# Kernel tuning notes

Measured on AMD Instinct MI355X. Metric: run time of the kernel, lower is better.

Reference implementation:

```python
import jax, jax.numpy as jnp
import numpy as np

N_USERS = 100000
N_ITEMS = 400000
N_NODES = N_USERS + N_ITEMS
EMB_DIM = 64
N_LAYERS = 3
N_EDGES = 1200000


def setup_inputs() -> dict:
    key = jax.random.key(0)
    k1, k2, k3, k4 = jax.random.split(key, 4)
    # Xavier-uniform init for embedding tables
    bound_u = float(np.sqrt(6.0 / (N_USERS + EMB_DIM)))
    bound_i = float(np.sqrt(6.0 / (N_ITEMS + EMB_DIM)))
    user_emb_w = jax.random.uniform(k1, (N_USERS, EMB_DIM), jnp.float32, -bound_u, bound_u)
    item_emb_w = jax.random.uniform(k2, (N_ITEMS, EMB_DIM), jnp.float32, -bound_i, bound_i)
    edge_index = jax.random.randint(k3, (2, N_EDGES), 0, N_NODES, dtype=jnp.int64)
    edge_weight = jax.random.uniform(k4, (N_EDGES,), jnp.float32)
    return {
        "user_emb_w": user_emb_w,
        "item_emb_w": item_emb_w,
        "edge_index": edge_index,
        "edge_weight": edge_weight,
    }


def _lgconv(x, src, dst, w):
    # gather source features, scale by edge weight, scatter-add to dst
    msgs = x[src] * w[:, None]              # [E, D]
    return jax.ops.segment_sum(msgs, dst, num_segments=N_NODES)  # [N, D]


def reference(user_emb_w, item_emb_w, edge_index, edge_weight):
    src, dst = edge_index[0], edge_index[1]
    x = jnp.concatenate([user_emb_w, item_emb_w], axis=0)  # [N, D]
    acc = x  # running sum of layer embeddings (fused stack+mean)
    for _ in range(N_LAYERS):
        x = _lgconv(x, src, dst, edge_weight)
        acc = acc + x
    final = acc / jnp.asarray(N_LAYERS + 1, x.dtype)
    return final[:N_USERS], final[N_USERS:]
```

## Files before the change

### kernel.cpp

```cpp
#include <hip/hip_runtime.h>

#define N_USERS 100000
#define N_ITEMS 400000
#define N_NODES 500000
#define EMB_DIM 64
#define N_EDGES 1200000

#define BUCK_SHIFT 11
#define BUCK_NODES 2048
#define NBUCK 245
#define BUCK_CAP 6144
#define CHUNK 4096

typedef long long ll;
typedef float f4 __attribute__((ext_vector_type(4)));
typedef float f8 __attribute__((ext_vector_type(8)));
typedef unsigned short u16;
typedef u16 us8 __attribute__((ext_vector_type(8)));

__device__ __forceinline__ u16 f2bf(float f) {
    unsigned u = __float_as_uint(f);
    u += 0x7FFF + ((u >> 16) & 1);
    return (u16)(u >> 16);
}
__device__ __forceinline__ float bf2f(u16 h) {
    return __uint_as_float(((unsigned)h) << 16);
}
__device__ __forceinline__ void fma8(f8& s, float w, us8 v) {
    #pragma unroll
    for (int k = 0; k < 8; ++k) s[k] += w * bf2f(v[k]);
}


__global__ void k_init(int* __restrict__ gcur) {
    if (threadIdx.x < 256) gcur[threadIdx.x] = 0;
}

__global__ void k_bsort(const int* __restrict__ src, const int* __restrict__ dst,
                        const float* __restrict__ w,
                        int* __restrict__ gcur, uint2* __restrict__ stage) {
    __shared__ int lhist[256];
    __shared__ int gbase_s[256];
    __shared__ int lcur[256];
    int tid = threadIdx.x;
    lhist[tid] = 0;
    __syncthreads();
    int c0 = blockIdx.x * CHUNK;
    int c1 = c0 + CHUNK < N_EDGES ? c0 + CHUNK : N_EDGES;
    #pragma unroll
    for (int r = 0; r < CHUNK / 256; ++r) {
        int e = c0 + r * 256 + tid;
        if (e < c1) atomicAdd(&lhist[dst[e] >> BUCK_SHIFT], 1);
    }
    __syncthreads();
    if (tid < NBUCK) {
        gbase_s[tid] = atomicAdd(&gcur[tid], lhist[tid]);
        lcur[tid] = 0;
    }
    __syncthreads();
    #pragma unroll
    for (int r = 0; r < CHUNK / 256; ++r) {
        int e = c0 + r * 256 + tid;
        if (e < c1) {
            int s = src[e];
            int d = dst[e];
            float wt = w[e];
            int b = d >> BUCK_SHIFT;
            int k = atomicAdd(&lcur[b], 1);
            ll idx = (ll)b * BUCK_CAP + gbase_s[b] + k;
            stage[idx] = make_uint2((unsigned)s | ((unsigned)(d & (BUCK_NODES - 1)) << 19),
                                    __float_as_uint(wt));
        }
    }
}

__global__ void k_ncount(const uint2* __restrict__ stage, const int* __restrict__ gcur,
                         int* __restrict__ counts) {
    __shared__ int lh[BUCK_NODES];
    int b = blockIdx.x;
    int tid = threadIdx.x;
    #pragma unroll
    for (int r = 0; r < BUCK_NODES / 256; ++r) lh[r * 256 + tid] = 0;
    __syncthreads();
    int cnt = gcur[b];
    const uint2* sb = stage + (ll)b * BUCK_CAP;
    for (int i = tid; i < cnt; i += 256)
        atomicAdd(&lh[(sb[i].x >> 19) & (BUCK_NODES - 1)], 1);
    __syncthreads();
    int nbase = b * BUCK_NODES;
    #pragma unroll
    for (int r = 0; r < BUCK_NODES / 256; ++r) {
        int i = r * 256 + tid;
        int n = nbase + i;
        if (n < N_NODES) counts[n] = lh[i];
    }
}

#define SCAN_ELEMS 1024
__global__ void k_scan1(int* __restrict__ data, int* __restrict__ blocksums) {
    __shared__ int tmp[256];
    int b = blockIdx.x;
    int t = threadIdx.x;
    int base = b * SCAN_ELEMS + t * 4;
    int v[4];
    #pragma unroll
    for (int k = 0; k < 4; ++k) {
        int i = base + k;
        v[k] = (i < N_NODES) ? data[i] : 0;
    }
    int tsum = v[0] + v[1] + v[2] + v[3];
    tmp[t] = tsum;
    __syncthreads();
    for (int off = 1; off < 256; off <<= 1) {
        int x = (t >= off) ? tmp[t - off] : 0;
        __syncthreads();
        tmp[t] += x;
        __syncthreads();
    }
    int run = tmp[t] - tsum;
    #pragma unroll
    for (int k = 0; k < 4; ++k) {
        int i = base + k;
        if (i < N_NODES) data[i] = run;
        run += v[k];
    }
    if (t == 255) blocksums[b] = tmp[255];
}

__global__ void k_scan2(int* __restrict__ blocksums, int nb) {
    __shared__ int tmp[512];
    int t = threadIdx.x;
    int v = (t < nb) ? blocksums[t] : 0;
    tmp[t] = v;
    __syncthreads();
    for (int off = 1; off < 512; off <<= 1) {
        int x = (t >= off) ? tmp[t - off] : 0;
        __syncthreads();
        tmp[t] += x;
        __syncthreads();
    }
    if (t < nb) blocksums[t] = tmp[t] - v;
}

__global__ void k_scan3(int* __restrict__ rowptr, const int* __restrict__ blocksums) {
    int stride = gridDim.x * blockDim.x;
    for (int i = blockIdx.x * blockDim.x + threadIdx.x; i < N_NODES; i += stride)
        rowptr[i] = rowptr[i] + blocksums[i >> 10];
    if (blockIdx.x == 0 && threadIdx.x == 0) rowptr[N_NODES] = N_EDGES;
}

__global__ void k_place(const uint2* __restrict__ stage, const int* __restrict__ gcur,
                        const int* __restrict__ rowptr, int2* __restrict__ csr) {
    __shared__ int lpos[BUCK_NODES];
    int b = blockIdx.x;
    int tid = threadIdx.x;
    int nbase = b * BUCK_NODES;
    #pragma unroll
    for (int r = 0; r < BUCK_NODES / 256; ++r) {
        int i = r * 256 + tid;
        int n = nbase + i;
        lpos[i] = (n < N_NODES) ? rowptr[n] : 0;
    }
    __syncthreads();
    int cnt = gcur[b];
    const uint2* sb = stage + (ll)b * BUCK_CAP;
    for (int i = tid; i < cnt; i += 256) {
        uint2 e = sb[i];
        int ldst = (e.x >> 19) & (BUCK_NODES - 1);
        int s = e.x & 0x7FFFF;
        int pos = atomicAdd(&lpos[ldst], 1);
        csr[pos] = make_int2(s, (int)e.y);
    }
}


__global__ void k_conv(const f4* __restrict__ u4, const f4* __restrict__ i4,
                       us8* __restrict__ x0b) {
    const int total = N_NODES * 8;
    const int user8 = N_USERS * 8;
    int stride = gridDim.x * blockDim.x;
    for (int i = blockIdx.x * blockDim.x + threadIdx.x; i < total; i += stride) {
        const f4* p = (i < user8) ? (u4 + (ll)i * 2) : (i4 + (ll)(i - user8) * 2);
        f4 lo = __builtin_nontemporal_load(p);
        f4 hi = __builtin_nontemporal_load(p + 1);
        us8 o;
        #pragma unroll
        for (int k = 0; k < 4; ++k) { o[k] = f2bf(lo[k]); o[k + 4] = f2bf(hi[k]); }
        x0b[i] = o;
    }
}


__device__ __forceinline__ f8 gather8(const us8* __restrict__ xin,
                                      const int* __restrict__ rowptr,
                                      const int2* __restrict__ csr,
                                      int n, int fl) {
    int start = rowptr[n];
    int end   = rowptr[n + 1];
    int deg = end - start;
    f8 s = {0.f, 0.f, 0.f, 0.f, 0.f, 0.f, 0.f, 0.f};
    if (deg > 0) {
        int lastj = end - 1;
        int j1 = start + 1 < end ? start + 1 : lastj;
        int j2 = start + 2 < end ? start + 2 : lastj;
        int j3 = start + 3 < end ? start + 3 : lastj;
        int2 e0 = csr[start];
        int2 e1 = csr[j1];
        int2 e2 = csr[j2];
        int2 e3 = csr[j3];
        float w0 = __int_as_float(e0.y);
        float w1 = (deg > 1) ? __int_as_float(e1.y) : 0.f;
        float w2 = (deg > 2) ? __int_as_float(e2.y) : 0.f;
        float w3 = (deg > 3) ? __int_as_float(e3.y) : 0.f;
        us8 v0 = xin[(ll)e0.x * 8 + fl];
        us8 v1 = xin[(ll)e1.x * 8 + fl];
        us8 v2 = xin[(ll)e2.x * 8 + fl];
        us8 v3 = xin[(ll)e3.x * 8 + fl];
        fma8(s, w0, v0);
        fma8(s, w1, v1);
        fma8(s, w2, v2);
        fma8(s, w3, v3);
        int j = start + 4;
        for (; j + 1 < end; j += 2) {
            int2 a = csr[j];
            int2 b = csr[j + 1];
            us8 va = xin[(ll)a.x * 8 + fl];
            us8 vb = xin[(ll)b.x * 8 + fl];
            fma8(s, __int_as_float(a.y), va);
            fma8(s, __int_as_float(b.y), vb);
        }
        if (j < end) {
            int2 a = csr[j];
            us8 va = xin[(ll)a.x * 8 + fl];
            fma8(s, __int_as_float(a.y), va);
        }
    }
    return s;
}

__global__ void k_prop(const us8* __restrict__ xin,
                       const int* __restrict__ rowptr,
                       const int2* __restrict__ csr,
                       us8* __restrict__ xout) {
    int wave = (blockIdx.x * blockDim.x + threadIdx.x) >> 6;
    int lane = threadIdx.x & 63;
    int sub = lane >> 3;
    int fl  = lane & 7;
    int nwaves = (gridDim.x * blockDim.x) >> 6;
    for (int nb = wave * 8; nb < N_NODES; nb += nwaves * 8) {
        int n = nb + sub;
        f8 s = gather8(xin, rowptr, csr, n, fl);
        us8 o;
        #pragma unroll
        for (int k = 0; k < 8; ++k) o[k] = f2bf(s[k]);
        xout[(ll)n * 8 + fl] = o;
    }
}

__global__ void k_final(const us8* __restrict__ x0b,
                        const us8* __restrict__ x1b, const us8* __restrict__ x2b,
                        const int* __restrict__ rowptr,
                        const int2* __restrict__ csr,
                        f4* __restrict__ acc) {
    int wave = (blockIdx.x * blockDim.x + threadIdx.x) >> 6;
    int lane = threadIdx.x & 63;
    int sub = lane >> 3;
    int fl  = lane & 7;
    int nwaves = (gridDim.x * blockDim.x) >> 6;
    for (int nb = wave * 8; nb < N_NODES; nb += nwaves * 8) {
        int n = nb + sub;
        f8 s = gather8(x2b, rowptr, csr, n, fl);
        ll idx8 = (ll)n * 8 + fl;
        us8 x0v = x0b[idx8];
        us8 x1v = __builtin_nontemporal_load(&x1b[idx8]);
        us8 x2v = x2b[idx8];
        f4 rlo, rhi;
        #pragma unroll
        for (int k = 0; k < 4; ++k)
            rlo[k] = 0.25f * (bf2f(x0v[k]) + bf2f(x1v[k]) + bf2f(x2v[k]) + s[k]);
        #pragma unroll
        for (int k = 0; k < 4; ++k)
            rhi[k] = 0.25f * (bf2f(x0v[k + 4]) + bf2f(x1v[k + 4]) + bf2f(x2v[k + 4]) + s[k + 4]);
        f4* arow = acc + (ll)n * 16;
        __builtin_nontemporal_store(rlo, &arow[fl * 2]);
        __builtin_nontemporal_store(rhi, &arow[fl * 2 + 1]);
    }
}


__global__ void fb_init(const float* __restrict__ user_w,
                        const float* __restrict__ item_w,
                        float* __restrict__ acc, float* __restrict__ xcur) {
    const ll total4 = (ll)N_NODES * EMB_DIM / 4;
    const ll user4 = (ll)N_USERS * EMB_DIM / 4;
    const float4* uw = (const float4*)user_w;
    const float4* iw = (const float4*)item_w;
    float4* a4 = (float4*)acc;
    float4* x4 = (float4*)xcur;
    ll stride = (ll)gridDim.x * blockDim.x;
    for (ll i = (ll)blockIdx.x * blockDim.x + threadIdx.x; i < total4; i += stride) {
        float4 v = (i < user4) ? uw[i] : iw[i - user4];
        x4[i] = v;
        a4[i] = make_float4(0.25f * v.x, 0.25f * v.y, 0.25f * v.z, 0.25f * v.w);
    }
}
__global__ void fb_zero(float* __restrict__ p) {
    const ll total4 = (ll)N_NODES * EMB_DIM / 4;
    float4* p4 = (float4*)p;
    ll stride = (ll)gridDim.x * blockDim.x;
    float4 z = make_float4(0.f, 0.f, 0.f, 0.f);
    for (ll i = (ll)blockIdx.x * blockDim.x + threadIdx.x; i < total4; i += stride)
        p4[i] = z;
}
__global__ void fb_scatter(const float* __restrict__ xcur, const int* __restrict__ src,
                           const int* __restrict__ dst, const float* __restrict__ w,
                           float* __restrict__ xnext) {
    const int gpb = blockDim.x >> 6;
    const int d = threadIdx.x & 63;
    int eg = blockIdx.x * gpb + (threadIdx.x >> 6);
    const int estride = gridDim.x * gpb;
    for (int e = eg; e < N_EDGES; e += estride) {
        int s = src[e]; int t = dst[e]; float wt = w[e];
        atomicAdd(&xnext[(ll)t * EMB_DIM + d], xcur[(ll)s * EMB_DIM + d] * wt);
    }
}
__global__ void fb_accadd(const float* __restrict__ xn, float* __restrict__ acc) {
    const ll total4 = (ll)N_NODES * EMB_DIM / 4;
    const float4* x4 = (const float4*)xn;
    float4* a4 = (float4*)acc;
    ll stride = (ll)gridDim.x * blockDim.x;
    for (ll i = (ll)blockIdx.x * blockDim.x + threadIdx.x; i < total4; i += stride) {
        float4 v = x4[i]; float4 a = a4[i];
        a.x += 0.25f * v.x; a.y += 0.25f * v.y;
        a.z += 0.25f * v.z; a.w += 0.25f * v.w;
        a4[i] = a;
    }
}


extern "C" void kernel_launch(void* const* d_in, const int* in_sizes, int n_in,
                              void* d_out, int out_size, void* d_ws, size_t ws_size,
                              hipStream_t stream) {
    const float* user_w = (const float*)d_in[0];
    const float* item_w = (const float*)d_in[1];
    const int*   eidx   = (const int*)d_in[2];
    const float* ew     = (const float*)d_in[3];
    const int* src = eidx;
    const int* dst = eidx + N_EDGES;

    const size_t xb_bf = (size_t)N_NODES * EMB_DIM * 2;
    size_t off = 0;
    size_t x0_off     = off;   off += xb_bf;
    size_t x1_off     = off;   off += xb_bf;
    size_t x2_off     = off;   off += xb_bf;
    size_t stage_off  = off;   off += (size_t)NBUCK * BUCK_CAP * 8;
    size_t csr_off    = off;   off += (size_t)N_EDGES * 8;
    size_t rowptr_off = off;   off += (size_t)(N_NODES + 1) * 4;
    size_t gcur_off   = off;   off += 256 * 4;
    size_t bsums_off  = off;   off += 4096;
    const size_t need = off;

    const int blk = 256;

    if (ws_size >= need) {
        us8*   x0b   = (us8*)((char*)d_ws + x0_off);
        us8*   x1b   = (us8*)((char*)d_ws + x1_off);
        us8*   x2b   = (us8*)((char*)d_ws + x2_off);
        uint2* stage = (uint2*)((char*)d_ws + stage_off);
        int2*  csr   = (int2*)((char*)d_ws + csr_off);
        int*   rowptr = (int*)((char*)d_ws + rowptr_off);
        int*   gcur   = (int*)((char*)d_ws + gcur_off);
        int*   bsums  = (int*)((char*)d_ws + bsums_off);
        f4*    acc    = (f4*)d_out;
        const f4* u4 = (const f4*)user_w;
        const f4* i4 = (const f4*)item_w;

        const int nb_scan = (N_NODES + SCAN_ELEMS - 1) / SCAN_ELEMS;
        const int nb_sort = (N_EDGES + CHUNK - 1) / CHUNK;

        k_init<<<1, 256, 0, stream>>>(gcur);
        k_bsort<<<nb_sort, blk, 0, stream>>>(src, dst, ew, gcur, stage);
        k_ncount<<<NBUCK, blk, 0, stream>>>(stage, gcur, rowptr);
        k_scan1<<<nb_scan, 256, 0, stream>>>(rowptr, bsums);
        k_scan2<<<1, 512, 0, stream>>>(bsums, nb_scan);
        k_scan3<<<2048, blk, 0, stream>>>(rowptr, bsums);
        k_place<<<NBUCK, blk, 0, stream>>>(stage, gcur, rowptr, csr);

        k_conv<<<2048, blk, 0, stream>>>(u4, i4, x0b);

        const int grid_l = 4096;
        k_prop<<<grid_l, blk, 0, stream>>>(x0b, rowptr, csr, x1b);
        k_prop<<<grid_l, blk, 0, stream>>>(x1b, rowptr, csr, x2b);
        k_final<<<grid_l, blk, 0, stream>>>(x0b, x1b, x2b, rowptr, csr, acc);
    } else {
        float* acc = (float*)d_out;
        float* xcur = (float*)d_ws;
        float* xnext = xcur + (ll)N_NODES * EMB_DIM;
        fb_init<<<2048, blk, 0, stream>>>(user_w, item_w, acc, xcur);
        for (int layer = 0; layer < 3; ++layer) {
            fb_zero<<<2048, blk, 0, stream>>>(xnext);
            fb_scatter<<<4096, blk, 0, stream>>>(xcur, src, dst, ew, xnext);
            fb_accadd<<<2048, blk, 0, stream>>>(xnext, acc);
            float* tmp = xcur; xcur = xnext; xnext = tmp;
        }
    }
}
```

Measured before the change: 244.1 us.

## Fuse embedding conversion into bucket sort and process two nodes per sub-wave

The fp32-to-bf16 conversion of the embedding tables now runs in extra blocks of the bucket-sort kernel, so the two independent jobs share one launch and can overlap. The propagation and final kernels now handle two destination nodes per 8-lane group, issuing the first four neighbour gathers for both nodes up front. This raises memory-level parallelism in the latency-bound gather and removes one launch. In exchange it uses more registers per thread, which may lower occupancy, and it adds clamped speculative CSR index loads.

```diff
diff --git a/kernel.cpp b/kernel.cpp
--- a/kernel.cpp
+++ b/kernel.cpp
@@ -11,6 +11,8 @@
 #define NBUCK 245
 #define BUCK_CAP 6144
 #define CHUNK 4096
+#define NB_SORT 293
+#define NB_CONV 1024
 
 typedef long long ll;
 typedef float f4 __attribute__((ext_vector_type(4)));
@@ -36,13 +38,33 @@
     if (threadIdx.x < 256) gcur[threadIdx.x] = 0;
 }
 
-__global__ void k_bsort(const int* __restrict__ src, const int* __restrict__ dst,
-                        const float* __restrict__ w,
-                        int* __restrict__ gcur, uint2* __restrict__ stage) {
+__global__ void k_bsort_conv(const int* __restrict__ src, const int* __restrict__ dst,
+                             const float* __restrict__ w,
+                             int* __restrict__ gcur, uint2* __restrict__ stage,
+                             const f4* __restrict__ u4, const f4* __restrict__ i4,
+                             us8* __restrict__ x0b) {
     __shared__ int lhist[256];
     __shared__ int gbase_s[256];
     __shared__ int lcur[256];
     int tid = threadIdx.x;
+
+    if (blockIdx.x >= NB_SORT) {
+        const int total = N_NODES * 8;
+        const int user8 = N_USERS * 8;
+        int i0 = (blockIdx.x - NB_SORT) * 256 + tid;
+        int stride = NB_CONV * 256;
+        for (int i = i0; i < total; i += stride) {
+            const f4* p = (i < user8) ? (u4 + (ll)i * 2) : (i4 + (ll)(i - user8) * 2);
+            f4 lo = __builtin_nontemporal_load(p);
+            f4 hi = __builtin_nontemporal_load(p + 1);
+            us8 o;
+            #pragma unroll
+            for (int k = 0; k < 4; ++k) { o[k] = f2bf(lo[k]); o[k + 4] = f2bf(hi[k]); }
+            x0b[i] = o;
+        }
+        return;
+    }
+
     lhist[tid] = 0;
     __syncthreads();
     int c0 = blockIdx.x * CHUNK;
@@ -174,68 +196,32 @@
 }
 
 
-__global__ void k_conv(const f4* __restrict__ u4, const f4* __restrict__ i4,
-                       us8* __restrict__ x0b) {
-    const int total = N_NODES * 8;
-    const int user8 = N_USERS * 8;
-    int stride = gridDim.x * blockDim.x;
-    for (int i = blockIdx.x * blockDim.x + threadIdx.x; i < total; i += stride) {
-        const f4* p = (i < user8) ? (u4 + (ll)i * 2) : (i4 + (ll)(i - user8) * 2);
-        f4 lo = __builtin_nontemporal_load(p);
-        f4 hi = __builtin_nontemporal_load(p + 1);
-        us8 o;
-        #pragma unroll
-        for (int k = 0; k < 4; ++k) { o[k] = f2bf(lo[k]); o[k + 4] = f2bf(hi[k]); }
-        x0b[i] = o;
-    }
-}
-
-
-__device__ __forceinline__ f8 gather8(const us8* __restrict__ xin,
-                                      const int* __restrict__ rowptr,
-                                      const int2* __restrict__ csr,
-                                      int n, int fl) {
-    int start = rowptr[n];
-    int end   = rowptr[n + 1];
-    int deg = end - start;
-    f8 s = {0.f, 0.f, 0.f, 0.f, 0.f, 0.f, 0.f, 0.f};
-    if (deg > 0) {
-        int lastj = end - 1;
-        int j1 = start + 1 < end ? start + 1 : lastj;
-        int j2 = start + 2 < end ? start + 2 : lastj;
-        int j3 = start + 3 < end ? start + 3 : lastj;
-        int2 e0 = csr[start];
-        int2 e1 = csr[j1];
-        int2 e2 = csr[j2];
-        int2 e3 = csr[j3];
-        float w0 = __int_as_float(e0.y);
-        float w1 = (deg > 1) ? __int_as_float(e1.y) : 0.f;
-        float w2 = (deg > 2) ? __int_as_float(e2.y) : 0.f;
-        float w3 = (deg > 3) ? __int_as_float(e3.y) : 0.f;
-        us8 v0 = xin[(ll)e0.x * 8 + fl];
-        us8 v1 = xin[(ll)e1.x * 8 + fl];
-        us8 v2 = xin[(ll)e2.x * 8 + fl];
-        us8 v3 = xin[(ll)e3.x * 8 + fl];
-        fma8(s, w0, v0);
-        fma8(s, w1, v1);
-        fma8(s, w2, v2);
-        fma8(s, w3, v3);
-        int j = start + 4;
-        for (; j + 1 < end; j += 2) {
-            int2 a = csr[j];
-            int2 b = csr[j + 1];
-            us8 va = xin[(ll)a.x * 8 + fl];
-            us8 vb = xin[(ll)b.x * 8 + fl];
-            fma8(s, __int_as_float(a.y), va);
-            fma8(s, __int_as_float(b.y), vb);
-        }
-        if (j < end) {
-            int2 a = csr[j];
-            us8 va = xin[(ll)a.x * 8 + fl];
-            fma8(s, __int_as_float(a.y), va);
-        }
-    }
-    return s;
+__device__ __forceinline__ void bidx4(int start, int end,
+                                      int& j0, int& j1, int& j2, int& j3) {
+    j0 = start < N_EDGES - 1 ? start : N_EDGES - 1;
+    int lastj = (end - 1 > start) ? end - 1 : j0;
+    j1 = start + 1 < end ? start + 1 : lastj;
+    j2 = start + 2 < end ? start + 2 : lastj;
+    j3 = start + 3 < end ? start + 3 : lastj;
+}
+
+__device__ __forceinline__ void rem4(const us8* __restrict__ xin,
+                                     const int2* __restrict__ csr,
+                                     int start, int end, int fl, f8& s) {
+    int j = start + 4;
+    for (; j + 1 < end; j += 2) {
+        int2 a = csr[j];
+        int2 b = csr[j + 1];
+        us8 va = xin[(ll)a.x * 8 + fl];
+        us8 vb = xin[(ll)b.x * 8 + fl];
+        fma8(s, __int_as_float(a.y), va);
+        fma8(s, __int_as_float(b.y), vb);
+    }
+    if (j < end) {
+        int2 a = csr[j];
+        us8 va = xin[(ll)a.x * 8 + fl];
+        fma8(s, __int_as_float(a.y), va);
+    }
 }
 
 __global__ void k_prop(const us8* __restrict__ xin,
@@ -247,13 +233,46 @@
     int sub = lane >> 3;
     int fl  = lane & 7;
     int nwaves = (gridDim.x * blockDim.x) >> 6;
-    for (int nb = wave * 8; nb < N_NODES; nb += nwaves * 8) {
-        int n = nb + sub;
-        f8 s = gather8(xin, rowptr, csr, n, fl);
-        us8 o;
+    for (int nb = wave * 16; nb < N_NODES; nb += nwaves * 16) {
+        int na = nb + sub;
+        int nc = nb + 8 + sub;
+        int sa = rowptr[na], ea = rowptr[na + 1];
+        int sc = rowptr[nc], ec = rowptr[nc + 1];
+        int dega = ea - sa, degc = ec - sc;
+        int ja0, ja1, ja2, ja3, jc0, jc1, jc2, jc3;
+        bidx4(sa, ea, ja0, ja1, ja2, ja3);
+        bidx4(sc, ec, jc0, jc1, jc2, jc3);
+        int2 a0 = csr[ja0], a1 = csr[ja1], a2 = csr[ja2], a3 = csr[ja3];
+        int2 c0 = csr[jc0], c1 = csr[jc1], c2 = csr[jc2], c3 = csr[jc3];
+        us8 va0 = xin[(ll)a0.x * 8 + fl];
+        us8 va1 = xin[(ll)a1.x * 8 + fl];
+        us8 va2 = xin[(ll)a2.x * 8 + fl];
+        us8 va3 = xin[(ll)a3.x * 8 + fl];
+        us8 vc0 = xin[(ll)c0.x * 8 + fl];
+        us8 vc1 = xin[(ll)c1.x * 8 + fl];
+        us8 vc2 = xin[(ll)c2.x * 8 + fl];
+        us8 vc3 = xin[(ll)c3.x * 8 + fl];
+        float wa0 = (dega > 0) ? __int_as_float(a0.y) : 0.f;
+        float wa1 = (dega > 1) ? __int_as_float(a1.y) : 0.f;
+        float wa2 = (dega > 2) ? __int_as_float(a2.y) : 0.f;
+        float wa3 = (dega > 3) ? __int_as_float(a3.y) : 0.f;
+        float wc0 = (degc > 0) ? __int_as_float(c0.y) : 0.f;
+        float wc1 = (degc > 1) ? __int_as_float(c1.y) : 0.f;
+        float wc2 = (degc > 2) ? __int_as_float(c2.y) : 0.f;
+        float wc3 = (degc > 3) ? __int_as_float(c3.y) : 0.f;
+        f8 s1 = {0.f, 0.f, 0.f, 0.f, 0.f, 0.f, 0.f, 0.f};
+        f8 s2 = {0.f, 0.f, 0.f, 0.f, 0.f, 0.f, 0.f, 0.f};
+        fma8(s1, wa0, va0); fma8(s1, wa1, va1);
+        fma8(s1, wa2, va2); fma8(s1, wa3, va3);
+        fma8(s2, wc0, vc0); fma8(s2, wc1, vc1);
+        fma8(s2, wc2, vc2); fma8(s2, wc3, vc3);
+        if (dega > 4) rem4(xin, csr, sa, ea, fl, s1);
+        if (degc > 4) rem4(xin, csr, sc, ec, fl, s2);
+        us8 o1, o2;
         #pragma unroll
-        for (int k = 0; k < 8; ++k) o[k] = f2bf(s[k]);
-        xout[(ll)n * 8 + fl] = o;
+        for (int k = 0; k < 8; ++k) { o1[k] = f2bf(s1[k]); o2[k] = f2bf(s2[k]); }
+        xout[(ll)na * 8 + fl] = o1;
+        xout[(ll)nc * 8 + fl] = o2;
     }
 }
 
@@ -267,21 +286,64 @@
     int sub = lane >> 3;
     int fl  = lane & 7;
     int nwaves = (gridDim.x * blockDim.x) >> 6;
-    for (int nb = wave * 8; nb < N_NODES; nb += nwaves * 8) {
-        int n = nb + sub;
-        f8 s = gather8(x2b, rowptr, csr, n, fl);
-        ll idx8 = (ll)n * 8 + fl;
-        us8 x0v = x0b[idx8];
-        us8 x1v = __builtin_nontemporal_load(&x1b[idx8]);
-        us8 x2v = x2b[idx8];
+    for (int nb = wave * 16; nb < N_NODES; nb += nwaves * 16) {
+        int na = nb + sub;
+        int nc = nb + 8 + sub;
+        int sa = rowptr[na], ea = rowptr[na + 1];
+        int sc = rowptr[nc], ec = rowptr[nc + 1];
+        int dega = ea - sa, degc = ec - sc;
+        int ja0, ja1, ja2, ja3, jc0, jc1, jc2, jc3;
+        bidx4(sa, ea, ja0, ja1, ja2, ja3);
+        bidx4(sc, ec, jc0, jc1, jc2, jc3);
+        int2 a0 = csr[ja0], a1 = csr[ja1], a2 = csr[ja2], a3 = csr[ja3];
+        int2 c0 = csr[jc0], c1 = csr[jc1], c2 = csr[jc2], c3 = csr[jc3];
+        ll ia = (ll)na * 8 + fl;
+        ll ic = (ll)nc * 8 + fl;
+        us8 va0 = x2b[(ll)a0.x * 8 + fl];
+        us8 va1 = x2b[(ll)a1.x * 8 + fl];
+        us8 va2 = x2b[(ll)a2.x * 8 + fl];
+        us8 va3 = x2b[(ll)a3.x * 8 + fl];
+        us8 vc0 = x2b[(ll)c0.x * 8 + fl];
+        us8 vc1 = x2b[(ll)c1.x * 8 + fl];
+        us8 vc2 = x2b[(ll)c2.x * 8 + fl];
+        us8 vc3 = x2b[(ll)c3.x * 8 + fl];
+        us8 x0a = x0b[ia];
+        us8 x1a = __builtin_nontemporal_load(&x1b[ia]);
+        us8 x2a = x2b[ia];
+        us8 x0c = x0b[ic];
+        us8 x1c = __builtin_nontemporal_load(&x1b[ic]);
+        us8 x2c = x2b[ic];
+        float wa0 = (dega > 0) ? __int_as_float(a0.y) : 0.f;
+        float wa1 = (dega > 1) ? __int_as_float(a1.y) : 0.f;
+        float wa2 = (dega > 2) ? __int_as_float(a2.y) : 0.f;
+        float wa3 = (dega > 3) ? __int_as_float(a3.y) : 0.f;
+        float wc0 = (degc > 0) ? __int_as_float(c0.y) : 0.f;
+        float wc1 = (degc > 1) ? __int_as_float(c1.y) : 0.f;
+        float wc2 = (degc > 2) ? __int_as_float(c2.y) : 0.f;
+        float wc3 = (degc > 3) ? __int_as_float(c3.y) : 0.f;
+        f8 s1 = {0.f, 0.f, 0.f, 0.f, 0.f, 0.f, 0.f, 0.f};
+        f8 s2 = {0.f, 0.f, 0.f, 0.f, 0.f, 0.f, 0.f, 0.f};
+        fma8(s1, wa0, va0); fma8(s1, wa1, va1);
+        fma8(s1, wa2, va2); fma8(s1, wa3, va3);
+        fma8(s2, wc0, vc0); fma8(s2, wc1, vc1);
+        fma8(s2, wc2, vc2); fma8(s2, wc3, vc3);
+        if (dega > 4) rem4(x2b, csr, sa, ea, fl, s1);
+        if (degc > 4) rem4(x2b, csr, sc, ec, fl, s2);
         f4 rlo, rhi;
         #pragma unroll
-        for (int k = 0; k < 4; ++k)
-            rlo[k] = 0.25f * (bf2f(x0v[k]) + bf2f(x1v[k]) + bf2f(x2v[k]) + s[k]);
+        for (int k = 0; k < 4; ++k) {
+            rlo[k] = 0.25f * (bf2f(x0a[k]) + bf2f(x1a[k]) + bf2f(x2a[k]) + s1[k]);
+            rhi[k] = 0.25f * (bf2f(x0a[k + 4]) + bf2f(x1a[k + 4]) + bf2f(x2a[k + 4]) + s1[k + 4]);
+        }
+        f4* arow = acc + (ll)na * 16;
+        __builtin_nontemporal_store(rlo, &arow[fl * 2]);
+        __builtin_nontemporal_store(rhi, &arow[fl * 2 + 1]);
         #pragma unroll
-        for (int k = 0; k < 4; ++k)
-            rhi[k] = 0.25f * (bf2f(x0v[k + 4]) + bf2f(x1v[k + 4]) + bf2f(x2v[k + 4]) + s[k + 4]);
-        f4* arow = acc + (ll)n * 16;
+        for (int k = 0; k < 4; ++k) {
+            rlo[k] = 0.25f * (bf2f(x0c[k]) + bf2f(x1c[k]) + bf2f(x2c[k]) + s2[k]);
+            rhi[k] = 0.25f * (bf2f(x0c[k + 4]) + bf2f(x1c[k + 4]) + bf2f(x2c[k + 4]) + s2[k + 4]);
+        }
+        arow = acc + (ll)nc * 16;
         __builtin_nontemporal_store(rlo, &arow[fl * 2]);
         __builtin_nontemporal_store(rhi, &arow[fl * 2 + 1]);
     }
@@ -376,17 +438,15 @@
         const f4* i4 = (const f4*)item_w;
 
         const int nb_scan = (N_NODES + SCAN_ELEMS - 1) / SCAN_ELEMS;
-        const int nb_sort = (N_EDGES + CHUNK - 1) / CHUNK;
 
         k_init<<<1, 256, 0, stream>>>(gcur);
-        k_bsort<<<nb_sort, blk, 0, stream>>>(src, dst, ew, gcur, stage);
+        k_bsort_conv<<<NB_SORT + NB_CONV, blk, 0, stream>>>(src, dst, ew, gcur,
+                                                            stage, u4, i4, x0b);
         k_ncount<<<NBUCK, blk, 0, stream>>>(stage, gcur, rowptr);
         k_scan1<<<nb_scan, 256, 0, stream>>>(rowptr, bsums);
         k_scan2<<<1, 512, 0, stream>>>(bsums, nb_scan);
         k_scan3<<<2048, blk, 0, stream>>>(rowptr, bsums);
         k_place<<<NBUCK, blk, 0, stream>>>(stage, gcur, rowptr, csr);
-
-        k_conv<<<2048, blk, 0, stream>>>(u4, i4, x0b);
 
         const int grid_l = 4096;
         k_prop<<<grid_l, blk, 0, stream>>>(x0b, rowptr, csr, x1b);
```

Result: faster. 237.0 us (-2.9%).

## Fuse CSR build stages and merge bf16 conversion into bucket sort kernel

Applied to the files above, without the earlier changes.

Folds the float-to-bf16 embedding conversion into the bucket-sort launch as extra blocks, and replaces the global per-node count plus three-kernel scan with a tiny bucket-level scan followed by a per-bucket local histogram/scan inside the placement kernel. The second propagation layer now also writes the partial accumulator (x0+x1+x2), so the final kernel only reads acc and adds its own gather. This removes several launches and full passes over the 500k-entry rowptr array. In exchange the final kernel does a read-modify-write of the fp32 output instead of reading two bf16 arrays, and the mid layer writes fp32 output it did not write before.

```diff
diff --git a/kernel.cpp b/kernel.cpp
--- a/kernel.cpp
+++ b/kernel.cpp
@@ -11,6 +11,8 @@
 #define NBUCK 245
 #define BUCK_CAP 6144
 #define CHUNK 4096
+#define NB_SORT 293
+#define NB_CONV 1024
 
 typedef long long ll;
 typedef float f4 __attribute__((ext_vector_type(4)));
@@ -36,13 +38,33 @@
     if (threadIdx.x < 256) gcur[threadIdx.x] = 0;
 }
 
-__global__ void k_bsort(const int* __restrict__ src, const int* __restrict__ dst,
-                        const float* __restrict__ w,
-                        int* __restrict__ gcur, uint2* __restrict__ stage) {
+__global__ void k_bsort_conv(const int* __restrict__ src, const int* __restrict__ dst,
+                             const float* __restrict__ w,
+                             int* __restrict__ gcur, uint2* __restrict__ stage,
+                             const f4* __restrict__ u4, const f4* __restrict__ i4,
+                             us8* __restrict__ x0b) {
     __shared__ int lhist[256];
     __shared__ int gbase_s[256];
     __shared__ int lcur[256];
     int tid = threadIdx.x;
+
+    if (blockIdx.x >= NB_SORT) {
+        const int total = N_NODES * 8;
+        const int user8 = N_USERS * 8;
+        int i0 = (blockIdx.x - NB_SORT) * 256 + tid;
+        int stride = NB_CONV * 256;
+        for (int i = i0; i < total; i += stride) {
+            const f4* p = (i < user8) ? (u4 + (ll)i * 2) : (i4 + (ll)(i - user8) * 2);
+            f4 lo = __builtin_nontemporal_load(p);
+            f4 hi = __builtin_nontemporal_load(p + 1);
+            us8 o;
+            #pragma unroll
+            for (int k = 0; k < 4; ++k) { o[k] = f2bf(lo[k]); o[k + 4] = f2bf(hi[k]); }
+            x0b[i] = o;
+        }
+        return;
+    }
+
     lhist[tid] = 0;
     __syncthreads();
     int c0 = blockIdx.x * CHUNK;
@@ -74,42 +96,12 @@
     }
 }
 
-__global__ void k_ncount(const uint2* __restrict__ stage, const int* __restrict__ gcur,
-                         int* __restrict__ counts) {
-    __shared__ int lh[BUCK_NODES];
-    int b = blockIdx.x;
-    int tid = threadIdx.x;
-    #pragma unroll
-    for (int r = 0; r < BUCK_NODES / 256; ++r) lh[r * 256 + tid] = 0;
-    __syncthreads();
-    int cnt = gcur[b];
-    const uint2* sb = stage + (ll)b * BUCK_CAP;
-    for (int i = tid; i < cnt; i += 256)
-        atomicAdd(&lh[(sb[i].x >> 19) & (BUCK_NODES - 1)], 1);
-    __syncthreads();
-    int nbase = b * BUCK_NODES;
-    #pragma unroll
-    for (int r = 0; r < BUCK_NODES / 256; ++r) {
-        int i = r * 256 + tid;
-        int n = nbase + i;
-        if (n < N_NODES) counts[n] = lh[i];
-    }
-}
-
-#define SCAN_ELEMS 1024
-__global__ void k_scan1(int* __restrict__ data, int* __restrict__ blocksums) {
+__global__ void k_bscan(const int* __restrict__ gcur, int* __restrict__ bbase,
+                        int* __restrict__ rowptr) {
     __shared__ int tmp[256];
-    int b = blockIdx.x;
     int t = threadIdx.x;
-    int base = b * SCAN_ELEMS + t * 4;
-    int v[4];
-    #pragma unroll
-    for (int k = 0; k < 4; ++k) {
-        int i = base + k;
-        v[k] = (i < N_NODES) ? data[i] : 0;
-    }
-    int tsum = v[0] + v[1] + v[2] + v[3];
-    tmp[t] = tsum;
+    int v = (t < NBUCK) ? gcur[t] : 0;
+    tmp[t] = v;
     __syncthreads();
     for (int off = 1; off < 256; off <<= 1) {
         int x = (t >= off) ? tmp[t - off] : 0;
@@ -117,76 +109,54 @@
         tmp[t] += x;
         __syncthreads();
     }
-    int run = tmp[t] - tsum;
-    #pragma unroll
-    for (int k = 0; k < 4; ++k) {
-        int i = base + k;
-        if (i < N_NODES) data[i] = run;
-        run += v[k];
-    }
-    if (t == 255) blocksums[b] = tmp[255];
-}
-
-__global__ void k_scan2(int* __restrict__ blocksums, int nb) {
-    __shared__ int tmp[512];
-    int t = threadIdx.x;
-    int v = (t < nb) ? blocksums[t] : 0;
-    tmp[t] = v;
-    __syncthreads();
-    for (int off = 1; off < 512; off <<= 1) {
-        int x = (t >= off) ? tmp[t - off] : 0;
-        __syncthreads();
-        tmp[t] += x;
-        __syncthreads();
-    }
-    if (t < nb) blocksums[t] = tmp[t] - v;
-}
-
-__global__ void k_scan3(int* __restrict__ rowptr, const int* __restrict__ blocksums) {
-    int stride = gridDim.x * blockDim.x;
-    for (int i = blockIdx.x * blockDim.x + threadIdx.x; i < N_NODES; i += stride)
-        rowptr[i] = rowptr[i] + blocksums[i >> 10];
-    if (blockIdx.x == 0 && threadIdx.x == 0) rowptr[N_NODES] = N_EDGES;
-}
-
-__global__ void k_place(const uint2* __restrict__ stage, const int* __restrict__ gcur,
-                        const int* __restrict__ rowptr, int2* __restrict__ csr) {
-    __shared__ int lpos[BUCK_NODES];
+    if (t < NBUCK) bbase[t] = tmp[t] - v;
+    if (t == 0) rowptr[N_NODES] = N_EDGES;
+}
+
+__global__ void k_place2(const uint2* __restrict__ stage, const int* __restrict__ gcur,
+                         const int* __restrict__ bbase,
+                         int* __restrict__ rowptr, int2* __restrict__ csr) {
+    __shared__ int lh[BUCK_NODES];
+    __shared__ int tsum[256];
     int b = blockIdx.x;
     int tid = threadIdx.x;
-    int nbase = b * BUCK_NODES;
-    #pragma unroll
-    for (int r = 0; r < BUCK_NODES / 256; ++r) {
-        int i = r * 256 + tid;
-        int n = nbase + i;
-        lpos[i] = (n < N_NODES) ? rowptr[n] : 0;
-    }
+    #pragma unroll
+    for (int r = 0; r < BUCK_NODES / 256; ++r) lh[r * 256 + tid] = 0;
     __syncthreads();
     int cnt = gcur[b];
     const uint2* sb = stage + (ll)b * BUCK_CAP;
+    for (int i = tid; i < cnt; i += 256)
+        atomicAdd(&lh[(sb[i].x >> 19) & (BUCK_NODES - 1)], 1);
+    __syncthreads();
+    int base_t = tid * 8;
+    int v[8];
+    int s = 0;
+    #pragma unroll
+    for (int k = 0; k < 8; ++k) { v[k] = lh[base_t + k]; s += v[k]; }
+    tsum[tid] = s;
+    __syncthreads();
+    for (int off = 1; off < 256; off <<= 1) {
+        int x = (tid >= off) ? tsum[tid - off] : 0;
+        __syncthreads();
+        tsum[tid] += x;
+        __syncthreads();
+    }
+    int run = bbase[b] + tsum[tid] - s;
+    int nbase = b * BUCK_NODES;
+    #pragma unroll
+    for (int k = 0; k < 8; ++k) {
+        int i = base_t + k;
+        int n = nbase + i;
+        if (n < N_NODES) rowptr[n] = run;
+        lh[i] = run;
+        run += v[k];
+    }
+    __syncthreads();
     for (int i = tid; i < cnt; i += 256) {
         uint2 e = sb[i];
         int ldst = (e.x >> 19) & (BUCK_NODES - 1);
-        int s = e.x & 0x7FFFF;
-        int pos = atomicAdd(&lpos[ldst], 1);
-        csr[pos] = make_int2(s, (int)e.y);
-    }
-}
-
-
-__global__ void k_conv(const f4* __restrict__ u4, const f4* __restrict__ i4,
-                       us8* __restrict__ x0b) {
-    const int total = N_NODES * 8;
-    const int user8 = N_USERS * 8;
-    int stride = gridDim.x * blockDim.x;
-    for (int i = blockIdx.x * blockDim.x + threadIdx.x; i < total; i += stride) {
-        const f4* p = (i < user8) ? (u4 + (ll)i * 2) : (i4 + (ll)(i - user8) * 2);
-        f4 lo = __builtin_nontemporal_load(p);
-        f4 hi = __builtin_nontemporal_load(p + 1);
-        us8 o;
-        #pragma unroll
-        for (int k = 0; k < 4; ++k) { o[k] = f2bf(lo[k]); o[k + 4] = f2bf(hi[k]); }
-        x0b[i] = o;
+        int pos = atomicAdd(&lh[ldst], 1);
+        csr[pos] = make_int2((int)(e.x & 0x7FFFF), (int)e.y);
     }
 }
 
@@ -257,11 +227,41 @@
     }
 }
 
-__global__ void k_final(const us8* __restrict__ x0b,
-                        const us8* __restrict__ x1b, const us8* __restrict__ x2b,
-                        const int* __restrict__ rowptr,
-                        const int2* __restrict__ csr,
-                        f4* __restrict__ acc) {
+__global__ void k_prop2_acc(const us8* __restrict__ x0b, const us8* __restrict__ x1b,
+                            const int* __restrict__ rowptr,
+                            const int2* __restrict__ csr,
+                            us8* __restrict__ x2b, f4* __restrict__ acc) {
+    int wave = (blockIdx.x * blockDim.x + threadIdx.x) >> 6;
+    int lane = threadIdx.x & 63;
+    int sub = lane >> 3;
+    int fl  = lane & 7;
+    int nwaves = (gridDim.x * blockDim.x) >> 6;
+    for (int nb = wave * 8; nb < N_NODES; nb += nwaves * 8) {
+        int n = nb + sub;
+        f8 s = gather8(x1b, rowptr, csr, n, fl);
+        ll idx8 = (ll)n * 8 + fl;
+        us8 o;
+        #pragma unroll
+        for (int k = 0; k < 8; ++k) o[k] = f2bf(s[k]);
+        x2b[idx8] = o;
+        us8 x0v = __builtin_nontemporal_load(&x0b[idx8]);
+        us8 x1v = x1b[idx8];
+        f4 rlo, rhi;
+        #pragma unroll
+        for (int k = 0; k < 4; ++k) {
+            rlo[k] = 0.25f * (bf2f(x0v[k]) + bf2f(x1v[k]) + s[k]);
+            rhi[k] = 0.25f * (bf2f(x0v[k + 4]) + bf2f(x1v[k + 4]) + s[k + 4]);
+        }
+        f4* arow = acc + (ll)n * 16;
+        arow[fl * 2] = rlo;
+        arow[fl * 2 + 1] = rhi;
+    }
+}
+
+__global__ void k_final3(const us8* __restrict__ x2b,
+                         const int* __restrict__ rowptr,
+                         const int2* __restrict__ csr,
+                         f4* __restrict__ acc) {
     int wave = (blockIdx.x * blockDim.x + threadIdx.x) >> 6;
     int lane = threadIdx.x & 63;
     int sub = lane >> 3;
@@ -270,20 +270,16 @@
     for (int nb = wave * 8; nb < N_NODES; nb += nwaves * 8) {
         int n = nb + sub;
         f8 s = gather8(x2b, rowptr, csr, n, fl);
-        ll idx8 = (ll)n * 8 + fl;
-        us8 x0v = x0b[idx8];
-        us8 x1v = __builtin_nontemporal_load(&x1b[idx8]);
-        us8 x2v = x2b[idx8];
-        f4 rlo, rhi;
+        f4* arow = acc + (ll)n * 16;
+        f4 alo = arow[fl * 2];
+        f4 ahi = arow[fl * 2 + 1];
         #pragma unroll
-        for (int k = 0; k < 4; ++k)
-            rlo[k] = 0.25f * (bf2f(x0v[k]) + bf2f(x1v[k]) + bf2f(x2v[k]) + s[k]);
-        #pragma unroll
-        for (int k = 0; k < 4; ++k)
-            rhi[k] = 0.25f * (bf2f(x0v[k + 4]) + bf2f(x1v[k + 4]) + bf2f(x2v[k + 4]) + s[k + 4]);
-        f4* arow = acc + (ll)n * 16;
-        __builtin_nontemporal_store(rlo, &arow[fl * 2]);
-        __builtin_nontemporal_store(rhi, &arow[fl * 2 + 1]);
+        for (int k = 0; k < 4; ++k) {
+            alo[k] += 0.25f * s[k];
+            ahi[k] += 0.25f * s[k + 4];
+        }
+        __builtin_nontemporal_store(alo, &arow[fl * 2]);
+        __builtin_nontemporal_store(ahi, &arow[fl * 2 + 1]);
     }
 }
 
@@ -356,8 +352,8 @@
     size_t stage_off  = off;   off += (size_t)NBUCK * BUCK_CAP * 8;
     size_t csr_off    = off;   off += (size_t)N_EDGES * 8;
     size_t rowptr_off = off;   off += (size_t)(N_NODES + 1) * 4;
-    size_t gcur_off   = off;   off += 256 * 4;
-    size_t bsums_off  = off;   off += 4096;
+    size_t gcur_off   = off;   off += 1024;
+    size_t bbase_off  = off;   off += 1024;
     const size_t need = off;
 
     const int blk = 256;
@@ -370,28 +366,21 @@
         int2*  csr   = (int2*)((char*)d_ws + csr_off);
         int*   rowptr = (int*)((char*)d_ws + rowptr_off);
         int*   gcur   = (int*)((char*)d_ws + gcur_off);
-        int*   bsums  = (int*)((char*)d_ws + bsums_off);
+        int*   bbase  = (int*)((char*)d_ws + bbase_off);
         f4*    acc    = (f4*)d_out;
         const f4* u4 = (const f4*)user_w;
         const f4* i4 = (const f4*)item_w;
 
-        const int nb_scan = (N_NODES + SCAN_ELEMS - 1) / SCAN_ELEMS;
-        const int nb_sort = (N_EDGES + CHUNK - 1) / CHUNK;
-
         k_init<<<1, 256, 0, stream>>>(gcur);
-        k_bsort<<<nb_sort, blk, 0, stream>>>(src, dst, ew, gcur, stage);
-        k_ncount<<<NBUCK, blk, 0, stream>>>(stage, gcur, rowptr);
-        k_scan1<<<nb_scan, 256, 0, stream>>>(rowptr, bsums);
-        k_scan2<<<1, 512, 0, stream>>>(bsums, nb_scan);
-        k_scan3<<<2048, blk, 0, stream>>>(rowptr, bsums);
-        k_place<<<NBUCK, blk, 0, stream>>>(stage, gcur, rowptr, csr);
-
-        k_conv<<<2048, blk, 0, stream>>>(u4, i4, x0b);
+        k_bsort_conv<<<NB_SORT + NB_CONV, blk, 0, stream>>>(src, dst, ew, gcur,
+                                                            stage, u4, i4, x0b);
+        k_bscan<<<1, 256, 0, stream>>>(gcur, bbase, rowptr);
+        k_place2<<<NBUCK, blk, 0, stream>>>(stage, gcur, bbase, rowptr, csr);
 
         const int grid_l = 4096;
         k_prop<<<grid_l, blk, 0, stream>>>(x0b, rowptr, csr, x1b);
-        k_prop<<<grid_l, blk, 0, stream>>>(x1b, rowptr, csr, x2b);
-        k_final<<<grid_l, blk, 0, stream>>>(x0b, x1b, x2b, rowptr, csr, acc);
+        k_prop2_acc<<<grid_l, blk, 0, stream>>>(x0b, x1b, rowptr, csr, x2b, acc);
+        k_final3<<<grid_l, blk, 0, stream>>>(x2b, rowptr, csr, acc);
     } else {
         float* acc = (float*)d_out;
         float* xcur = (float*)d_ws;
```

New measurement: 278.6 us. +14.1%, slower.
